# Performance work log

Hardware: AMD Instinct MI355X
Metric: run time of the kernel (lower is better)

Reference implementation:

```python
import jax, jax.numpy as jnp
import numpy as np

D_MODEL = 1024
N_HEAD = 16
D_HEAD = D_MODEL // N_HEAD


def setup_inputs() -> dict:
    key = jax.random.key(0)
    ks = jax.random.split(key, 12)
    L, B, M = 2048, 2, 2048
    s = 1.0 / np.sqrt(D_MODEL)
    return {
        "q": jax.random.normal(ks[0], (L, B, D_MODEL), jnp.float32),
        "kv": jax.random.normal(ks[1], (L, B, D_MODEL), jnp.float32),
        "mem": jax.random.normal(ks[2], (M, B, D_MODEL), jnp.float32),
        "w_q": jax.random.normal(ks[3], (D_MODEL, D_MODEL), jnp.float32) * s,
        "b_q": jnp.zeros((D_MODEL,), jnp.float32),
        "w_k": jax.random.normal(ks[4], (D_MODEL, D_MODEL), jnp.float32) * s,
        "b_k": jnp.zeros((D_MODEL,), jnp.float32),
        "w_v": jax.random.normal(ks[5], (D_MODEL, D_MODEL), jnp.float32) * s,
        "b_v": jnp.zeros((D_MODEL,), jnp.float32),
        "w_c": jax.random.normal(ks[6], (D_MODEL, D_MODEL), jnp.float32) * s,
        "b_c": jnp.zeros((D_MODEL,), jnp.float32),
    }


def reference(q, kv, mem, w_q, b_q, w_k, b_k, w_v, b_v, w_c, b_c):
    # c: [L+M, B, D]
    c = jnp.concatenate([mem, kv], axis=0)
    L, B, _ = q.shape
    J = c.shape[0]
    # linear projections (torch Linear: x @ W^T + b)
    qh = (q @ w_q.T + b_q).reshape(L, B, N_HEAD, D_HEAD)
    kh = (c @ w_k.T + b_k).reshape(J, B, N_HEAD, D_HEAD)
    vh = (c @ w_v.T + b_v).reshape(J, B, N_HEAD, D_HEAD)
    # attention scores [i, j, b, n]
    score = jnp.einsum("ibnd,jbnd->ijbn", qh, kh) / np.sqrt(D_HEAD).astype(np.float32)
    prob = jax.nn.softmax(score, axis=1)
    vec = jnp.einsum("ijbn,jbnd->ibnd", prob, vh).reshape(L, B, D_MODEL)
    return vec @ w_c.T + b_c
```

## Files before the change

### kernel.cpp

```cpp
#include <hip/hip_runtime.h>


using short8 = __attribute__((ext_vector_type(8))) short;
using f32x4  = __attribute__((ext_vector_type(4))) float;

#define DEV __device__ __forceinline__

DEV unsigned short f2bf(float f) {
  union { float f; unsigned int u; } x; x.f = f;
  unsigned int r = x.u + 0x7FFFu + ((x.u >> 16) & 1u);
  return (unsigned short)(r >> 16);
}

DEV unsigned int cvtpk(float lo, float hi) {
  unsigned int r;
  asm("v_cvt_pk_bf16_f32 %0, %1, %2" : "=v"(r) : "v"(lo), "v"(hi));
  return r;
}

DEV void gload_lds16(const unsigned short* g, unsigned short* l) {
  __builtin_amdgcn_global_load_lds(
      (const __attribute__((address_space(1))) unsigned int*)g,
      (__attribute__((address_space(3))) unsigned int*)l, 16, 0, 0);
}

__global__ __launch_bounds__(256) void convert_all(
    const float* __restrict__ q, const float* __restrict__ mem_,
    const float* __restrict__ kv, const float* __restrict__ wq,
    const float* __restrict__ wk, const float* __restrict__ wv,
    const float* __restrict__ wc, unsigned short* __restrict__ a_bf,
    unsigned short* __restrict__ c_bf, unsigned short* __restrict__ w_bf) {
  size_t u = (size_t)blockIdx.x * 256 + threadIdx.x;
  const float* src;
  unsigned short* dst;
  if (u < 524288u)        { src = q    + u * 8;                dst = a_bf + u * 8; }
  else if (u < 1048576u)  { src = mem_ + (u - 524288u) * 8;    dst = c_bf + (u - 524288u) * 8; }
  else if (u < 1572864u)  { src = kv   + (u - 1048576u) * 8;   dst = c_bf + 4194304u + (u - 1048576u) * 8; }
  else if (u < 1703936u)  { src = wq   + (u - 1572864u) * 8;   dst = w_bf + (u - 1572864u) * 8; }
  else if (u < 1835008u)  { src = wk   + (u - 1703936u) * 8;   dst = w_bf + 1048576u + (u - 1703936u) * 8; }
  else if (u < 1966080u)  { src = wv   + (u - 1835008u) * 8;   dst = w_bf + 2097152u + (u - 1835008u) * 8; }
  else                    { src = wc   + (u - 1966080u) * 8;   dst = w_bf + 3145728u + (u - 1966080u) * 8; }
  float4 v0 = ((const float4*)src)[0];
  float4 v1 = ((const float4*)src)[1];
  union { unsigned short us[8]; uint4 v; } o;
  o.us[0] = f2bf(v0.x); o.us[1] = f2bf(v0.y); o.us[2] = f2bf(v0.z); o.us[3] = f2bf(v0.w);
  o.us[4] = f2bf(v1.x); o.us[5] = f2bf(v1.y); o.us[6] = f2bf(v1.z); o.us[7] = f2bf(v1.w);
  *(uint4*)dst = o.v;
}

template <int MODE>
__global__ __launch_bounds__(256, 2) void gemm_bt(
    const unsigned short* __restrict__ A, const unsigned short* __restrict__ Bw,
    const float* __restrict__ bias, void* __restrict__ outp) {
  __shared__ __align__(16) unsigned short lA[128 * 64];
  __shared__ __align__(16) unsigned short lB[128 * 64];
  const int tid = threadIdx.x;
  const int lane = tid & 63;
  const int w = tid >> 6;
  const int wr = w >> 1, wcn = w & 1;
  const int tm = blockIdx.x * 128;
  const int tn = blockIdx.y * 128;

  const int srow = lane >> 3;
  const int scol = ((lane & 7) ^ srow) * 8;
  const unsigned short* aptr = A + (size_t)(tm + 32 * w + srow) * 1024 + scol;
  const unsigned short* bptr = Bw + (size_t)(tn + 32 * w + srow) * 1024 + scol;
  unsigned short* lAw = &lA[(32 * w) * 64];
  unsigned short* lBw = &lB[(32 * w) * 64];

  const f32x4 zero = {0.f, 0.f, 0.f, 0.f};
  f32x4 acc[4][4];
#pragma unroll
  for (int i = 0; i < 4; ++i)
#pragma unroll
    for (int j = 0; j < 4; ++j) acc[i][j] = zero;

  for (int kb = 0; kb < 16; ++kb) {
    const int ko = kb * 64;
#pragma unroll
    for (int c = 0; c < 4; ++c) {
      gload_lds16(aptr + ko + c * 8 * 1024, lAw + c * 8 * 64);
      gload_lds16(bptr + ko + c * 8 * 1024, lBw + c * 8 * 64);
    }
    __syncthreads();
#pragma unroll
    for (int kk = 0; kk < 2; ++kk) {
      short8 af[4], bfr[4];
#pragma unroll
      for (int mi = 0; mi < 4; ++mi) {
        int r = 64 * wr + 16 * mi + (lane & 15);
        int slot = (kk * 4 + (lane >> 4)) ^ (r & 7);
        af[mi] = *(const short8*)&lA[r * 64 + slot * 8];
      }
#pragma unroll
      for (int ni = 0; ni < 4; ++ni) {
        int r = 64 * wcn + 16 * ni + (lane & 15);
        int slot = (kk * 4 + (lane >> 4)) ^ (r & 7);
        bfr[ni] = *(const short8*)&lB[r * 64 + slot * 8];
      }
#pragma unroll
      for (int mi = 0; mi < 4; ++mi)
#pragma unroll
        for (int ni = 0; ni < 4; ++ni)
          acc[mi][ni] = __builtin_amdgcn_mfma_f32_16x16x32_bf16(
              af[mi], bfr[ni], acc[mi][ni], 0, 0, 0);
    }
    __syncthreads();
  }

  const int g4 = (lane >> 4) * 4;
  const int c0 = lane & 15;
#pragma unroll
  for (int mi = 0; mi < 4; ++mi) {
#pragma unroll
    for (int ni = 0; ni < 4; ++ni) {
      const int colt = tn + 64 * wcn + 16 * ni + c0;
      const float bv = bias[colt];
#pragma unroll
      for (int j = 0; j < 4; ++j) {
        const int rowt = tm + 64 * wr + 16 * mi + g4 + j;
        const float v = acc[mi][ni][j] + bv;
        if constexpr (MODE == 0) {
          ((float*)outp)[(size_t)rowt * 1024 + colt] = v;
        } else if constexpr (MODE == 1) {
          const int i = rowt >> 1, b = rowt & 1, n = colt >> 6, d = colt & 63;
          ((unsigned short*)outp)[(((size_t)(b * 16 + n) * 2048 + i) << 6) + d] =
              f2bf(v * 0.1803368801111f);
        } else if constexpr (MODE == 2) {
          const int jj = rowt >> 1, b = rowt & 1, n = colt >> 6, d = colt & 63;
          ((unsigned short*)outp)[(((size_t)(b * 16 + n) * 4096 + jj) << 6) + d] = f2bf(v);
        } else {
          const int jj = rowt >> 1, b = rowt & 1, n = colt >> 6, d = colt & 63;
          const int j6 = jj & 63;
          const int pos = (j6 & 3) | (((j6 >> 4) & 1) << 2) | (((j6 >> 2) & 3) << 3) |
                          (((j6 >> 5) & 1) << 5);
          ((unsigned short*)outp)[((size_t)(b * 16 + n) * 64 + d) * 4096 + (jj & ~63) + pos] =
              f2bf(v);
        }
      }
    }
  }
}

__global__ __launch_bounds__(512, 2) void attn_kernel(
    const unsigned short* __restrict__ qh, const unsigned short* __restrict__ kh,
    const unsigned short* __restrict__ vt, unsigned short* __restrict__ vec) {
  __shared__ __align__(16) unsigned short kl[2][64 * 64];
  __shared__ __align__(16) unsigned short vl[2][64 * 64];
  const int tid = threadIdx.x;
  const int lane = tid & 63;
  const int w = tid >> 6;
  const int g = lane >> 4;
  const int l4 = lane & 15;
  const int f = blockIdx.x;
  const int head = (f & 7) * 4 + ((f >> 3) & 3);
  const int qt = f >> 5;
  const int b = head >> 4, n = head & 15;
  const unsigned short* qbase = qh + ((size_t)head * 2048 + qt * 256 + 32 * w) * 64;
  const unsigned short* kbase = kh + (size_t)head * 4096 * 64;
  const unsigned short* vbase = vt + (size_t)head * 64 * 4096;

  short8 qf[2][2];
#pragma unroll
  for (int mi = 0; mi < 2; ++mi)
#pragma unroll
    for (int kk = 0; kk < 2; ++kk)
      qf[mi][kk] = *(const short8*)&qbase[(16 * mi + l4) * 64 + kk * 32 + g * 8];

  const f32x4 zero = {0.f, 0.f, 0.f, 0.f};
  f32x4 oacc[2][4];
#pragma unroll
  for (int mi = 0; mi < 2; ++mi)
#pragma unroll
    for (int nd = 0; nd < 4; ++nd) oacc[mi][nd] = zero;
  float mrow[2] = {-3.0e38f, -3.0e38f};
  float lrow[2] = {0.f, 0.f};

  const int srow = lane >> 3;
  const int scol = ((lane & 7) ^ srow) * 8;
  const unsigned short* kp = kbase + (size_t)(8 * w + srow) * 64 + scol;
  const unsigned short* vp = vbase + (size_t)(8 * w + srow) * 4096 + scol;

  auto stage = [&](int jt, int bufi) {
    gload_lds16(kp + (size_t)jt * 4096, &kl[bufi][(8 * w) * 64]);
    gload_lds16(vp + jt * 64, &vl[bufi][(8 * w) * 64]);
  };

  stage(0, 0);
  __syncthreads();

  for (int jt = 0; jt < 64; ++jt) {
    const int buf = jt & 1;
    if (jt < 63) stage(jt + 1, buf ^ 1);

    f32x4 s[2][4];
#pragma unroll
    for (int mi = 0; mi < 2; ++mi)
#pragma unroll
      for (int nj = 0; nj < 4; ++nj) s[mi][nj] = zero;
#pragma unroll
    for (int kk = 0; kk < 2; ++kk) {
      short8 bk[4];
#pragma unroll
      for (int nj = 0; nj < 4; ++nj) {
        int r = 16 * nj + l4;
        int slot = (kk * 4 + g) ^ (r & 7);
        bk[nj] = *(const short8*)&kl[buf][r * 64 + slot * 8];
      }
#pragma unroll
      for (int mi = 0; mi < 2; ++mi)
#pragma unroll
        for (int nj = 0; nj < 4; ++nj)
          s[mi][nj] = __builtin_amdgcn_mfma_f32_16x16x32_bf16(bk[nj], qf[mi][kk], s[mi][nj], 0, 0, 0);
    }

    short8 pa[2][2];
#pragma unroll
    for (int mi = 0; mi < 2; ++mi) {
      float a0 = fmaxf(fmaxf(s[mi][0][0], s[mi][0][1]), fmaxf(s[mi][0][2], s[mi][0][3]));
      float a1 = fmaxf(fmaxf(s[mi][1][0], s[mi][1][1]), fmaxf(s[mi][1][2], s[mi][1][3]));
      float a2 = fmaxf(fmaxf(s[mi][2][0], s[mi][2][1]), fmaxf(s[mi][2][2], s[mi][2][3]));
      float a3 = fmaxf(fmaxf(s[mi][3][0], s[mi][3][1]), fmaxf(s[mi][3][2], s[mi][3][3]));
      float pmax = fmaxf(fmaxf(a0, a1), fmaxf(a2, a3));
      pmax = fmaxf(pmax, __shfl_xor(pmax, 16));
      pmax = fmaxf(pmax, __shfl_xor(pmax, 32));
      if (!__all(pmax <= mrow[mi] + 8.f)) {
        const float mnew = fmaxf(mrow[mi], pmax);
        const float sc = __builtin_amdgcn_exp2f(mrow[mi] - mnew);
        mrow[mi] = mnew;
        lrow[mi] *= sc;
#pragma unroll
        for (int reg = 0; reg < 4; ++reg) {
          const float scr = __shfl(sc, 4 * g + reg);
#pragma unroll
          for (int nd = 0; nd < 4; ++nd) oacc[mi][nd][reg] *= scr;
        }
      }
      const float m = mrow[mi];
      float rs = 0.f;
#pragma unroll
      for (int nj = 0; nj < 4; ++nj)
#pragma unroll
        for (int reg = 0; reg < 4; ++reg) {
          const float p = __builtin_amdgcn_exp2f(s[mi][nj][reg] - m);
          s[mi][nj][reg] = p;
          rs += p;
        }
      rs += __shfl_xor(rs, 16);
      rs += __shfl_xor(rs, 32);
      lrow[mi] += rs;
#pragma unroll
      for (int kk2 = 0; kk2 < 2; ++kk2) {
        union { unsigned int u[4]; short8 v; } t;
#pragma unroll
        for (int wd = 0; wd < 4; ++wd) {
          const int nj = (wd >> 1) + 2 * kk2;
          const int r0 = (wd & 1) * 2;
          t.u[wd] = cvtpk(s[mi][nj][r0], s[mi][nj][r0 + 1]);
        }
        pa[mi][kk2] = t.v;
      }
    }

#pragma unroll
    for (int kk2 = 0; kk2 < 2; ++kk2) {
      short8 bv4[4];
#pragma unroll
      for (int nd = 0; nd < 4; ++nd) {
        const int r = 16 * nd + l4;
        const int blk = (g + 4 * kk2) ^ (r & 7);
        bv4[nd] = *(const short8*)&vl[buf][r * 64 + blk * 8];
      }
#pragma unroll
      for (int mi = 0; mi < 2; ++mi)
#pragma unroll
        for (int nd = 0; nd < 4; ++nd)
          oacc[mi][nd] = __builtin_amdgcn_mfma_f32_16x16x32_bf16(pa[mi][kk2], bv4[nd], oacc[mi][nd], 0, 0, 0);
    }
    __syncthreads();
  }

#pragma unroll
  for (int mi = 0; mi < 2; ++mi) {
#pragma unroll
    for (int reg = 0; reg < 4; ++reg) {
      const float lr = __shfl(lrow[mi], 4 * g + reg);
      const float inv = 1.f / lr;
      const int i = qt * 256 + 32 * w + 16 * mi + 4 * g + reg;
#pragma unroll
      for (int nd = 0; nd < 4; ++nd) {
        const int d = 16 * nd + l4;
        vec[(size_t)(i * 2 + b) * 1024 + n * 64 + d] = f2bf(oacc[mi][nd][reg] * inv);
      }
    }
  }
}

extern "C" void kernel_launch(void* const* d_in, const int* in_sizes, int n_in,
                              void* d_out, int out_size, void* d_ws, size_t ws_size,
                              hipStream_t stream) {
  (void)in_sizes; (void)n_in; (void)out_size; (void)ws_size;
  const float* q    = (const float*)d_in[0];
  const float* kv   = (const float*)d_in[1];
  const float* mem_ = (const float*)d_in[2];
  const float* wq   = (const float*)d_in[3];
  const float* bq   = (const float*)d_in[4];
  const float* wk   = (const float*)d_in[5];
  const float* bk   = (const float*)d_in[6];
  const float* wv   = (const float*)d_in[7];
  const float* bv   = (const float*)d_in[8];
  const float* wc   = (const float*)d_in[9];
  const float* bc   = (const float*)d_in[10];

  char* ws = (char*)d_ws;
  unsigned short* w_bf = (unsigned short*)(ws);
  unsigned short* a_bf = (unsigned short*)(ws + (8ull << 20));
  unsigned short* c_bf = (unsigned short*)(ws + (16ull << 20));
  unsigned short* qhb  = (unsigned short*)(ws + (32ull << 20));
  unsigned short* khb  = (unsigned short*)(ws + (40ull << 20));
  unsigned short* vtb  = (unsigned short*)(ws + (56ull << 20));
  unsigned short* vecb = a_bf;

  convert_all<<<8192, 256, 0, stream>>>(q, mem_, kv, wq, wk, wv, wc, a_bf, c_bf, w_bf);
  gemm_bt<1><<<dim3(32, 8), 256, 0, stream>>>(a_bf, w_bf,                bq, qhb);
  gemm_bt<2><<<dim3(64, 8), 256, 0, stream>>>(c_bf, w_bf + (1u << 20),   bk, khb);
  gemm_bt<3><<<dim3(64, 8), 256, 0, stream>>>(c_bf, w_bf + (2u << 20),   bv, vtb);
  attn_kernel<<<256, 512, 0, stream>>>(qhb, khb, vtb, vecb);
  gemm_bt<0><<<dim3(32, 8), 256, 0, stream>>>(vecb, w_bf + (3u << 20),   bc, d_out);
}
```

Before: 202.0 us.

## Restructure attention into 4-wave blocks with paired K/V tiles and deferred row sums

```diff
diff --git a/kernel.cpp b/kernel.cpp
--- a/kernel.cpp
+++ b/kernel.cpp
@@ -18,11 +18,24 @@
   return r;
 }
 
+DEV float max3f(float a, float b, float c) {
+  float d;
+  asm("v_max3_f32 %0, %1, %2, %3" : "=v"(d) : "v"(a), "v"(b), "v"(c));
+  return d;
+}
+
 DEV void gload_lds16(const unsigned short* g, unsigned short* l) {
   __builtin_amdgcn_global_load_lds(
       (const __attribute__((address_space(1))) unsigned int*)g,
       (__attribute__((address_space(3))) unsigned int*)l, 16, 0, 0);
 }
+
+#define BARRIER_RAW()                      \
+  do {                                     \
+    __builtin_amdgcn_sched_barrier(0);     \
+    __builtin_amdgcn_s_barrier();          \
+    __builtin_amdgcn_sched_barrier(0);     \
+  } while (0)
 
 __global__ __launch_bounds__(256) void convert_all(
     const float* __restrict__ q, const float* __restrict__ mem_,
@@ -142,11 +155,11 @@
   }
 }
 
-__global__ __launch_bounds__(512, 2) void attn_kernel(
+__global__ __launch_bounds__(256, 2) void attn_kernel(
     const unsigned short* __restrict__ qh, const unsigned short* __restrict__ kh,
     const unsigned short* __restrict__ vt, unsigned short* __restrict__ vec) {
-  __shared__ __align__(16) unsigned short kl[2][64 * 64];
-  __shared__ __align__(16) unsigned short vl[2][64 * 64];
+  __shared__ __align__(16) unsigned short kl[2][2][64 * 64];
+  __shared__ __align__(16) unsigned short vl[2][2][64 * 64];
   const int tid = threadIdx.x;
   const int lane = tid & 63;
   const int w = tid >> 6;
@@ -156,7 +169,7 @@
   const int head = (f & 7) * 4 + ((f >> 3) & 3);
   const int qt = f >> 5;
   const int b = head >> 4, n = head & 15;
-  const unsigned short* qbase = qh + ((size_t)head * 2048 + qt * 256 + 32 * w) * 64;
+  const unsigned short* qbase = qh + ((size_t)head * 2048 + qt * 128 + 32 * w) * 64;
   const unsigned short* kbase = kh + (size_t)head * 4096 * 64;
   const unsigned short* vbase = vt + (size_t)head * 64 * 4096;
 
@@ -174,30 +187,33 @@
 #pragma unroll
     for (int nd = 0; nd < 4; ++nd) oacc[mi][nd] = zero;
   float mrow[2] = {-3.0e38f, -3.0e38f};
-  float lrow[2] = {0.f, 0.f};
+  float lsum[2] = {0.f, 0.f};
 
   const int srow = lane >> 3;
   const int scol = ((lane & 7) ^ srow) * 8;
-  const unsigned short* kp = kbase + (size_t)(8 * w + srow) * 64 + scol;
-  const unsigned short* vp = vbase + (size_t)(8 * w + srow) * 4096 + scol;
-
-  auto stage = [&](int jt, int bufi) {
-    gload_lds16(kp + (size_t)jt * 4096, &kl[bufi][(8 * w) * 64]);
-    gload_lds16(vp + jt * 64, &vl[bufi][(8 * w) * 64]);
+  const unsigned short* kp = kbase + (size_t)(16 * w + srow) * 64 + scol;
+  const unsigned short* vp = vbase + (size_t)(16 * w + srow) * 4096 + scol;
+
+  auto stage_pair = [&](int jp, int bufi) {
+#pragma unroll
+    for (int sub = 0; sub < 2; ++sub) {
+      gload_lds16(kp + (size_t)jp * 8192 + sub * 4096,
+                  &kl[bufi][sub][(16 * w) * 64]);
+      gload_lds16(kp + (size_t)jp * 8192 + sub * 4096 + 8 * 64,
+                  &kl[bufi][sub][(16 * w + 8) * 64]);
+      gload_lds16(vp + jp * 128 + sub * 64, &vl[bufi][sub][(16 * w) * 64]);
+      gload_lds16(vp + jp * 128 + sub * 64 + 8 * 4096,
+                  &vl[bufi][sub][(16 * w + 8) * 64]);
+    }
   };
 
-  stage(0, 0);
-  __syncthreads();
-
-  for (int jt = 0; jt < 64; ++jt) {
-    const int buf = jt & 1;
-    if (jt < 63) stage(jt + 1, buf ^ 1);
-
+  auto subtile = [&](const unsigned short* kbuf, const unsigned short* vbuf) {
     f32x4 s[2][4];
 #pragma unroll
     for (int mi = 0; mi < 2; ++mi)
 #pragma unroll
       for (int nj = 0; nj < 4; ++nj) s[mi][nj] = zero;
+    __builtin_amdgcn_s_setprio(1);
 #pragma unroll
     for (int kk = 0; kk < 2; ++kk) {
       short8 bk[4];
@@ -205,7 +221,7 @@
       for (int nj = 0; nj < 4; ++nj) {
         int r = 16 * nj + l4;
         int slot = (kk * 4 + g) ^ (r & 7);
-        bk[nj] = *(const short8*)&kl[buf][r * 64 + slot * 8];
+        bk[nj] = *(const short8*)&kbuf[r * 64 + slot * 8];
       }
 #pragma unroll
       for (int mi = 0; mi < 2; ++mi)
@@ -213,22 +229,30 @@
         for (int nj = 0; nj < 4; ++nj)
           s[mi][nj] = __builtin_amdgcn_mfma_f32_16x16x32_bf16(bk[nj], qf[mi][kk], s[mi][nj], 0, 0, 0);
     }
-
-    short8 pa[2][2];
+    __builtin_amdgcn_s_setprio(0);
+
+    float pm[2];
 #pragma unroll
     for (int mi = 0; mi < 2; ++mi) {
-      float a0 = fmaxf(fmaxf(s[mi][0][0], s[mi][0][1]), fmaxf(s[mi][0][2], s[mi][0][3]));
-      float a1 = fmaxf(fmaxf(s[mi][1][0], s[mi][1][1]), fmaxf(s[mi][1][2], s[mi][1][3]));
-      float a2 = fmaxf(fmaxf(s[mi][2][0], s[mi][2][1]), fmaxf(s[mi][2][2], s[mi][2][3]));
-      float a3 = fmaxf(fmaxf(s[mi][3][0], s[mi][3][1]), fmaxf(s[mi][3][2], s[mi][3][3]));
-      float pmax = fmaxf(fmaxf(a0, a1), fmaxf(a2, a3));
-      pmax = fmaxf(pmax, __shfl_xor(pmax, 16));
-      pmax = fmaxf(pmax, __shfl_xor(pmax, 32));
-      if (!__all(pmax <= mrow[mi] + 8.f)) {
-        const float mnew = fmaxf(mrow[mi], pmax);
+      float t0 = max3f(s[mi][0][0], s[mi][0][1], s[mi][0][2]);
+      float t1 = max3f(s[mi][0][3], s[mi][1][0], s[mi][1][1]);
+      float t2 = max3f(s[mi][1][2], s[mi][1][3], s[mi][2][0]);
+      float t3 = max3f(s[mi][2][1], s[mi][2][2], s[mi][2][3]);
+      float t4 = max3f(s[mi][3][0], s[mi][3][1], s[mi][3][2]);
+      float p5 = max3f(t0, t1, t2);
+      p5 = max3f(p5, t3, t4);
+      pm[mi] = fmaxf(p5, s[mi][3][3]);
+    }
+    float pj = fmaxf(pm[0], pm[1]);
+    pj = fmaxf(pj, __shfl_xor(pj, 16));
+    pj = fmaxf(pj, __shfl_xor(pj, 32));
+    if (!__all(pj <= fminf(mrow[0], mrow[1]) + 8.f)) {
+#pragma unroll
+      for (int mi = 0; mi < 2; ++mi) {
+        const float mnew = fmaxf(mrow[mi], pj);
         const float sc = __builtin_amdgcn_exp2f(mrow[mi] - mnew);
         mrow[mi] = mnew;
-        lrow[mi] *= sc;
+        lsum[mi] *= sc;
 #pragma unroll
         for (int reg = 0; reg < 4; ++reg) {
           const float scr = __shfl(sc, 4 * g + reg);
@@ -236,6 +260,11 @@
           for (int nd = 0; nd < 4; ++nd) oacc[mi][nd][reg] *= scr;
         }
       }
+    }
+
+    short8 pa[2][2];
+#pragma unroll
+    for (int mi = 0; mi < 2; ++mi) {
       const float m = mrow[mi];
       float rs = 0.f;
 #pragma unroll
@@ -246,9 +275,7 @@
           s[mi][nj][reg] = p;
           rs += p;
         }
-      rs += __shfl_xor(rs, 16);
-      rs += __shfl_xor(rs, 32);
-      lrow[mi] += rs;
+      lsum[mi] += rs;
 #pragma unroll
       for (int kk2 = 0; kk2 < 2; ++kk2) {
         union { unsigned int u[4]; short8 v; } t;
@@ -262,6 +289,7 @@
       }
     }
 
+    __builtin_amdgcn_s_setprio(1);
 #pragma unroll
     for (int kk2 = 0; kk2 < 2; ++kk2) {
       short8 bv4[4];
@@ -269,7 +297,7 @@
       for (int nd = 0; nd < 4; ++nd) {
         const int r = 16 * nd + l4;
         const int blk = (g + 4 * kk2) ^ (r & 7);
-        bv4[nd] = *(const short8*)&vl[buf][r * 64 + blk * 8];
+        bv4[nd] = *(const short8*)&vbuf[r * 64 + blk * 8];
       }
 #pragma unroll
       for (int mi = 0; mi < 2; ++mi)
@@ -277,16 +305,38 @@
         for (int nd = 0; nd < 4; ++nd)
           oacc[mi][nd] = __builtin_amdgcn_mfma_f32_16x16x32_bf16(pa[mi][kk2], bv4[nd], oacc[mi][nd], 0, 0, 0);
     }
-    __syncthreads();
+    __builtin_amdgcn_s_setprio(0);
+  };
+
+  stage_pair(0, 0);
+  asm volatile("s_waitcnt vmcnt(0)" ::: "memory");
+  BARRIER_RAW();
+
+  for (int t2 = 0; t2 < 16; ++t2) {
+    stage_pair(2 * t2 + 1, 1);
+    subtile(kl[0][0], vl[0][0]);
+    subtile(kl[0][1], vl[0][1]);
+    asm volatile("s_waitcnt vmcnt(0)" ::: "memory");
+    BARRIER_RAW();
+    if (t2 < 15) stage_pair(2 * t2 + 2, 0);
+    subtile(kl[1][0], vl[1][0]);
+    subtile(kl[1][1], vl[1][1]);
+    if (t2 < 15) {
+      asm volatile("s_waitcnt vmcnt(0)" ::: "memory");
+      BARRIER_RAW();
+    }
   }
 
 #pragma unroll
   for (int mi = 0; mi < 2; ++mi) {
+    float l = lsum[mi];
+    l += __shfl_xor(l, 16);
+    l += __shfl_xor(l, 32);
 #pragma unroll
     for (int reg = 0; reg < 4; ++reg) {
-      const float lr = __shfl(lrow[mi], 4 * g + reg);
+      const float lr = __shfl(l, 4 * g + reg);
       const float inv = 1.f / lr;
-      const int i = qt * 256 + 32 * w + 16 * mi + 4 * g + reg;
+      const int i = qt * 128 + 32 * w + 16 * mi + 4 * g + reg;
 #pragma unroll
       for (int nd = 0; nd < 4; ++nd) {
         const int d = 16 * nd + l4;
@@ -325,6 +375,6 @@
   gemm_bt<1><<<dim3(32, 8), 256, 0, stream>>>(a_bf, w_bf,                bq, qhb);
   gemm_bt<2><<<dim3(64, 8), 256, 0, stream>>>(c_bf, w_bf + (1u << 20),   bk, khb);
   gemm_bt<3><<<dim3(64, 8), 256, 0, stream>>>(c_bf, w_bf + (2u << 20),   bv, vtb);
-  attn_kernel<<<256, 512, 0, stream>>>(qhb, khb, vtb, vecb);
+  attn_kernel<<<512, 256, 0, stream>>>(qhb, khb, vtb, vecb);
   gemm_bt<0><<<dim3(32, 8), 256, 0, stream>>>(vecb, w_bf + (3u << 20),   bc, d_out);
 }
```

Result: faster. 189.6 us (-6.1%).
